# Kernel optimization log

Hardware: AMD Instinct MI355X
Metric: run time of the kernel (lower is better)

## Reference

```python
import jax, jax.numpy as jnp
import numpy as np
import math

D_MODEL = 512
D_STATE = 16
D_CONV = 4
EXPAND = 2
D_INNER = EXPAND * D_MODEL
DT_RANK = math.ceil(D_MODEL / 16)
B_SZ, L_SEQ = 4, 4096


def setup_inputs() -> dict:
    key = jax.random.key(0)
    ks = jax.random.split(key, 32)
    f32 = jnp.float32

    def nrm(k, shape, s=0.02):
        return (jax.random.normal(k, shape, dtype=f32) * s)

    # dt bias init (inverse softplus of dt in [dt_min, dt_max])
    def dt_bias(k):
        u = jax.random.uniform(k, (D_INNER,), dtype=f32)
        dt = jnp.exp(u * (math.log(0.1) - math.log(1e-3)) + math.log(1e-3))
        dt = jnp.clip(dt, 1e-4, None)
        return dt + jnp.log(-jnp.expm1(-dt))

    Alog = jnp.log(jnp.broadcast_to(jnp.arange(1, D_STATE + 1, dtype=f32), (D_INNER, D_STATE)))
    dt_std = DT_RANK ** (-0.5)

    inp = {
        'hidden_states': jax.random.normal(ks[0], (B_SZ, L_SEQ, D_MODEL), dtype=f32),
        'another_hidden_states': jax.random.normal(ks[1], (B_SZ, L_SEQ, D_MODEL), dtype=f32),
        'in_proj_w': nrm(ks[2], (2 * D_INNER, D_MODEL)),
        'in_proj_g_w': nrm(ks[3], (2 * D_INNER, D_MODEL)),
        'convw_f': nrm(ks[4], (D_INNER, D_CONV), 0.1),
        'convb_f': jnp.zeros((D_INNER,), f32),
        'convw_r': nrm(ks[5], (D_INNER, D_CONV), 0.1),
        'convb_r': jnp.zeros((D_INNER,), f32),
        'convw_g': nrm(ks[6], (D_INNER, D_CONV), 0.1),
        'convb_g': jnp.zeros((D_INNER,), f32),
        'xproj_f': nrm(ks[7], (DT_RANK + 2 * D_STATE, D_INNER)),
        'xproj_r': nrm(ks[8], (DT_RANK + 2 * D_STATE, D_INNER)),
        'xproj_g': nrm(ks[9], (DT_RANK + 2 * D_STATE, D_INNER)),
        'dtw_f': jax.random.uniform(ks[10], (D_INNER, DT_RANK), minval=-dt_std, maxval=dt_std, dtype=f32),
        'dtb_f': dt_bias(ks[11]),
        'dtw_r': jax.random.uniform(ks[12], (D_INNER, DT_RANK), minval=-dt_std, maxval=dt_std, dtype=f32),
        'dtb_r': dt_bias(ks[13]),
        'dtw_g': jax.random.uniform(ks[14], (D_INNER, DT_RANK), minval=-dt_std, maxval=dt_std, dtype=f32),
        'dtb_g': dt_bias(ks[15]),
        'Alog_f': Alog, 'Alog_r': Alog, 'Alog_g': Alog,
        'D_f': jnp.ones((D_INNER,), f32),
        'D_r': jnp.ones((D_INNER,), f32),
        'D_g': jnp.ones((D_INNER,), f32),
        'out_proj_w': nrm(ks[16], (D_MODEL, D_INNER)),
    }
    return inp


def _branch(xz, convw, convb, xproj, dtw, dtb, Alog, Dp):
    # xz: (B, L, 2*d_inner)
    b, l, _ = xz.shape
    d = xz.shape[-1] // 2
    x, z = xz[..., :d], xz[..., d:]
    # causal depthwise conv1d over L (pad left d_conv-1), then SiLU
    xc = jnp.transpose(x, (0, 2, 1))  # (B, d, L)
    xc = jax.lax.conv_general_dilated(
        xc, convw[:, None, :], (1,), [(convw.shape[-1] - 1, 0)],
        dimension_numbers=('NCH', 'OIH', 'NCH'), feature_group_count=d)
    xc = xc + convb[None, :, None]
    x = jax.nn.silu(jnp.transpose(xc, (0, 2, 1)))  # (B, L, d)
    # input-dependent dt, B, C
    dbl = x @ xproj.T  # (B, L, dt_rank + 2n)
    r = dtw.shape[1]
    n = Alog.shape[1]
    dt = jax.nn.softplus(dbl[..., :r] @ dtw.T + dtb)  # (B, L, d)
    Bs = dbl[..., r:r + n]   # (B, L, n)
    Cs = dbl[..., r + n:]    # (B, L, n)
    A = -jnp.exp(Alog)       # (d, n)

    def step(h, inp):
        dt_t, x_t, B_t, C_t = inp  # (B,d),(B,d),(B,n),(B,n)
        h = jnp.exp(dt_t[:, :, None] * A) * h + (dt_t * x_t)[:, :, None] * B_t[:, None, :]
        y = jnp.einsum('bdn,bn->bd', h, C_t)
        return h, y

    h0 = jnp.zeros((b, d, n), dtype=x.dtype)
    xs = (jnp.swapaxes(dt, 0, 1), jnp.swapaxes(x, 0, 1),
          jnp.swapaxes(Bs, 0, 1), jnp.swapaxes(Cs, 0, 1))
    _, ys = jax.lax.scan(step, h0, xs)
    y = jnp.swapaxes(ys, 0, 1) + Dp * x  # (B, L, d)
    return y * jax.nn.silu(z)


def reference(hidden_states, another_hidden_states, in_proj_w, in_proj_g_w,
              convw_f, convb_f, convw_r, convb_r, convw_g, convb_g,
              xproj_f, xproj_r, xproj_g,
              dtw_f, dtb_f, dtw_r, dtb_r, dtw_g, dtb_g,
              Alog_f, Alog_r, Alog_g, D_f, D_r, D_g, out_proj_w):
    xz = hidden_states @ in_proj_w.T           # (B, L, 2*d_inner)
    axz = another_hidden_states @ in_proj_g_w.T
    y_f = _branch(xz, convw_f, convb_f, xproj_f, dtw_f, dtb_f, Alog_f, D_f)
    y_r = jnp.flip(_branch(jnp.flip(xz, axis=1), convw_r, convb_r, xproj_r, dtw_r, dtb_r, Alog_r, D_r), axis=1)
    y_g = _branch(axz, convw_g, convb_g, xproj_g, dtw_g, dtb_g, Alog_g, D_g)
    out = ((y_f + y_r) * jax.nn.silu(y_g)) @ out_proj_w.T  # (B, L, d_model)
    return out
```

## Files before the change

kernel.cpp:

```cpp
#include <hip/hip_runtime.h>
#include <hip/hip_bf16.h>
#include <math.h>

#define L_SEQ 4096
#define B_SZ 4
#define D_MODEL 512
#define D_INNER 1024
#define DT_RANK 32
#define D_STATE 16
#define M_ROWS (B_SZ * L_SEQ)
#define NC 64
#define CHK (L_SEQ / NC)

typedef __hip_bfloat16 bf16;
typedef __bf16 bf16x8 __attribute__((ext_vector_type(8)));
typedef float f32x4 __attribute__((ext_vector_type(4)));
struct us8 { ushort4 a, b; };

__device__ __forceinline__ unsigned short f2us(float f) {
    union { bf16 h; unsigned short u; } t;
    t.h = __float2bfloat16(f);
    return t.u;
}
__device__ __forceinline__ float us2f(unsigned short u) {
    union { bf16 h; unsigned short u; } t;
    t.u = u;
    return __bfloat162float(t.h);
}

__device__ __forceinline__ float silu_f(float x) {
    const float xc = fminf(fmaxf(x, -60.0f), 60.0f);
    return x / (1.0f + __expf(-xc));
}
__device__ __forceinline__ float softplus_f(float x) {
    if (x > 20.0f) return x;
    if (x < -20.0f) return __expf(x);
    return log1pf(__expf(x));
}

struct CvtArgs {
    const float* src[9];
    unsigned short* dst[9];
    unsigned int vend[9];
    int nseg;
};
__global__ __launch_bounds__(256)
void cvt_multi(CvtArgs a)
{
    const unsigned int v = blockIdx.x * 256 + threadIdx.x;
    if (v >= a.vend[a.nseg - 1]) return;
    int s = 0;
    unsigned int vstart = 0;
    while (v >= a.vend[s]) { vstart = a.vend[s]; ++s; }
    const size_t lv = (size_t)(v - vstart) * 4;
    const float4 f = *(const float4*)(a.src[s] + lv);
    ushort4 o;
    o.x = f2us(f.x); o.y = f2us(f.y); o.z = f2us(f.z); o.w = f2us(f.w);
    *(ushort4*)(a.dst[s] + lv) = o;
}

template<int BM, int BN, int BK, int WY, int WX, int GATED, int EPI, int CT, int SWZ>
__global__ __launch_bounds__(256)
void gemm_mfma(const unsigned short* __restrict__ A,
               const unsigned short* __restrict__ A2,
               const unsigned short* __restrict__ W,
               const float* __restrict__ bias,
               void* __restrict__ Cp, unsigned short* __restrict__ C2p,
               int K, int lda, int ldb, int ldc)
{
    constexpr int CPR = BK / 8;
    constexpr int SWM = CPR - 1;
    constexpr int RPW = 64 / CPR;
    constexpr int NPA = BM / (4 * RPW);
    constexpr int NPB = BN / (4 * RPW);
    constexpr int WGX = BN / (WX * 16);
    static_assert(WGX * (BM / (WY * 16)) == 4, "4 waves");
    __shared__ unsigned short As[BM * BK];
    __shared__ unsigned short Bs[BN * BK];

    const int tid  = threadIdx.x;
    const int lane = tid & 63;
    const int wave = tid >> 6;
    const int wx = wave % WGX, wy = wave / WGX;
    const int l15 = lane & 15, quad = lane >> 4;

    int bid = blockIdx.y * gridDim.x + blockIdx.x;
    if (SWZ) {
        const int nwg = gridDim.x * gridDim.y;
        if ((nwg & 7) == 0) {
            const int cpx = nwg >> 3;
            bid = (bid & 7) * cpx + (bid >> 3);
        }
    }
    const int bxi = bid % gridDim.x;
    const int byi = bid / gridDim.x;
    const long row0 = (long)byi * BM;
    const long col0 = (long)bxi * BN;

    const int rin = lane / CPR;
    const int gc  = (lane % CPR) ^ (rin & SWM);

    f32x4 acc[WY][WX];
#pragma unroll
    for (int i = 0; i < WY; ++i)
#pragma unroll
        for (int j = 0; j < WX; ++j) acc[i][j] = (f32x4){0.f, 0.f, 0.f, 0.f};

    for (int k0 = 0; k0 < K; k0 += BK) {
        if (GATED == 0) {
#pragma unroll
            for (int p = 0; p < NPA; ++p) {
                const int rb = (p * 4 + wave) * RPW;
                const unsigned short* gp = A + (row0 + rb + rin) * (long)lda + k0 + gc * 8;
                const int lb = __builtin_amdgcn_readfirstlane(rb * BK);
                __builtin_amdgcn_global_load_lds(
                    (const __attribute__((address_space(1))) void*)gp,
                    (__attribute__((address_space(3))) void*)(As + lb), 16, 0, 0);
            }
        } else {
#pragma unroll
            for (int v = 0; v < BM * BK / 2048; ++v) {
                const int e = (v * 256 + tid) * 8;
                const int r = e / BK, c = (e % BK) / 8;
                const long off = (row0 + r) * (long)lda + k0 + c * 8;
                const us8 ta = *(const us8*)(A + off);
                const us8 tg = *(const us8*)(A2 + off);
                us8 t;
                t.a.x = f2us(us2f(ta.a.x) * silu_f(us2f(tg.a.x)));
                t.a.y = f2us(us2f(ta.a.y) * silu_f(us2f(tg.a.y)));
                t.a.z = f2us(us2f(ta.a.z) * silu_f(us2f(tg.a.z)));
                t.a.w = f2us(us2f(ta.a.w) * silu_f(us2f(tg.a.w)));
                t.b.x = f2us(us2f(ta.b.x) * silu_f(us2f(tg.b.x)));
                t.b.y = f2us(us2f(ta.b.y) * silu_f(us2f(tg.b.y)));
                t.b.z = f2us(us2f(ta.b.z) * silu_f(us2f(tg.b.z)));
                t.b.w = f2us(us2f(ta.b.w) * silu_f(us2f(tg.b.w)));
                *(us8*)&As[r * BK + ((c ^ (r & SWM)) * 8)] = t;
            }
        }
#pragma unroll
        for (int p = 0; p < NPB; ++p) {
            const int rb = (p * 4 + wave) * RPW;
            const unsigned short* gp = W + (col0 + rb + rin) * (long)ldb + k0 + gc * 8;
            const int lb = __builtin_amdgcn_readfirstlane(rb * BK);
            __builtin_amdgcn_global_load_lds(
                (const __attribute__((address_space(1))) void*)gp,
                (__attribute__((address_space(3))) void*)(Bs + lb), 16, 0, 0);
        }
        __syncthreads();

#pragma unroll
        for (int kk = 0; kk < BK / 32; ++kk) {
            bf16x8 aF[WY], bF[WX];
#pragma unroll
            for (int i = 0; i < WY; ++i) {
                const int r  = wy * WY * 16 + i * 16 + l15;
                const int kc = (kk * 4 + quad) ^ (r & SWM);
                aF[i] = *(const bf16x8*)&As[r * BK + kc * 8];
            }
#pragma unroll
            for (int j = 0; j < WX; ++j) {
                const int r  = wx * WX * 16 + j * 16 + l15;
                const int kc = (kk * 4 + quad) ^ (r & SWM);
                bF[j] = *(const bf16x8*)&Bs[r * BK + kc * 8];
            }
#pragma unroll
            for (int i = 0; i < WY; ++i)
#pragma unroll
                for (int j = 0; j < WX; ++j)
                    acc[i][j] = __builtin_amdgcn_mfma_f32_16x16x32_bf16(
                        aF[i], bF[j], acc[i][j], 0, 0, 0);
        }
        __syncthreads();
    }

#pragma unroll
    for (int i = 0; i < WY; ++i)
#pragma unroll
        for (int j = 0; j < WX; ++j) {
            const long mb = row0 + wy * WY * 16 + i * 16 + quad * 4;
            const long n  = col0 + wx * WX * 16 + j * 16 + l15;
            const float bv = (EPI == 1) ? bias[n] : 0.0f;
#pragma unroll
            for (int r = 0; r < 4; ++r) {
                float val = acc[i][j][r];
                if (EPI == 1) val = softplus_f(val + bv);
                const long off = (mb + r) * (long)ldc + n;
                if (CT == 0) ((unsigned short*)Cp)[off] = f2us(val);
                else         ((float*)Cp)[off] = val;
                if (EPI == 2 && n < DT_RANK) C2p[(mb + r) * DT_RANK + n] = f2us(val);
            }
        }
}

__global__ __launch_bounds__(256)
void conv_silu8(const unsigned short* __restrict__ xz, const float* __restrict__ w,
                const float* __restrict__ bias, unsigned short* __restrict__ xb, int rev)
{
    const int idx = blockIdx.x * 256 + threadIdx.x;
    const int g = idx & 127;
    const int m = idx >> 7;
    const int b = m >> 12;
    const int t = m & (L_SEQ - 1);
    const int d = g * 8;

    float s[8];
    {
        const float4 b0 = *(const float4*)(bias + d);
        const float4 b1 = *(const float4*)(bias + d + 4);
        s[0] = b0.x; s[1] = b0.y; s[2] = b0.z; s[3] = b0.w;
        s[4] = b1.x; s[5] = b1.y; s[6] = b1.z; s[7] = b1.w;
    }
    float4 wv[8];
#pragma unroll
    for (int j = 0; j < 8; ++j) wv[j] = *(const float4*)(w + (d + j) * 4);

    const unsigned short* xbase = xz + (size_t)b * L_SEQ * 2048 + d;
#pragma unroll
    for (int k = 0; k < 4; ++k) {
        const int src = t - 3 + k;
        if (src >= 0) {
            const int sm = rev ? (L_SEQ - 1 - src) : src;
            const us8 xv = *(const us8*)(xbase + (size_t)sm * 2048);
            const float tap[8] = {us2f(xv.a.x), us2f(xv.a.y), us2f(xv.a.z), us2f(xv.a.w),
                                  us2f(xv.b.x), us2f(xv.b.y), us2f(xv.b.z), us2f(xv.b.w)};
#pragma unroll
            for (int j = 0; j < 8; ++j) {
                const float wk = (k == 0) ? wv[j].x : (k == 1) ? wv[j].y
                               : (k == 2) ? wv[j].z : wv[j].w;
                s[j] = fmaf(wk, tap[j], s[j]);
            }
        }
    }
    us8 o;
    o.a.x = f2us(silu_f(s[0])); o.a.y = f2us(silu_f(s[1]));
    o.a.z = f2us(silu_f(s[2])); o.a.w = f2us(silu_f(s[3]));
    o.b.x = f2us(silu_f(s[4])); o.b.y = f2us(silu_f(s[5]));
    o.b.z = f2us(silu_f(s[6])); o.b.w = f2us(silu_f(s[7]));
    *(us8*)(xb + (size_t)m * 1024 + d) = o;
}

__device__ __forceinline__ bool a_struct_fast(const float* __restrict__ Alog,
                                              int d, float& A0)
{
    A0 = -__expf(Alog[d * 16]);
    bool fast = true;
#pragma unroll
    for (int n = 1; n < 16; ++n) {
        const float an = -__expf(Alog[d * 16 + n]);
        const float tg = (float)(n + 1) * A0;
        fast = fast && (fabsf(an - tg) <= 1e-5f * fabsf(tg));
    }
    return fast;
}
__device__ __forceinline__ void pow_tree16(float e1, float w[16])
{
    w[0] = e1;
    w[1] = w[0] * w[0];  w[2] = w[1] * w[0];  w[3] = w[1] * w[1];
    w[4] = w[3] * w[0];  w[5] = w[3] * w[1];  w[6] = w[3] * w[2];  w[7] = w[3] * w[3];
#pragma unroll
    for (int n = 8; n < 16; ++n) w[n] = w[7] * w[n - 8];
}

__global__ __launch_bounds__(512)
void scan_a(const unsigned short* __restrict__ dtq, const unsigned short* __restrict__ xq,
            const float* __restrict__ dbl, const float* __restrict__ Alog,
            float* __restrict__ hF, float* __restrict__ Ssum)
{
    const int tid = threadIdx.x;
    const int d = blockIdx.y * 512 + tid;
    const int c = blockIdx.x;
    const int b = blockIdx.z;

    __shared__ float Bsh[CHK][16];
    for (int e = tid; e < CHK * 16; e += 512)
        Bsh[e >> 4][e & 15] = dbl[((size_t)b * L_SEQ + c * CHK + (e >> 4)) * 64 + DT_RANK + (e & 15)];
    __syncthreads();

    float A0;
    const bool fast = a_struct_fast(Alog, d, A0);

    float h[16];
#pragma unroll
    for (int n = 0; n < 16; ++n) h[n] = 0.0f;
    float S = 0.0f;

    const size_t base = ((size_t)b * L_SEQ + c * CHK) * 1024 + d;
    const unsigned short* dtp = dtq + base;
    const unsigned short* xp  = xq + base;

    if (fast) {
        unsigned short bd[4], bx[4];
#pragma unroll
        for (int i = 0; i < 4; ++i) {
            bd[i] = dtp[(size_t)i * 1024];
            bx[i] = xp[(size_t)i * 1024];
        }
        for (int t0 = 0; t0 < CHK; t0 += 4) {
            unsigned short nd[4], nx[4];
            const bool pf = (t0 + 4 < CHK);
            if (pf) {
#pragma unroll
                for (int i = 0; i < 4; ++i) {
                    nd[i] = dtp[(size_t)(t0 + 4 + i) * 1024];
                    nx[i] = xp[(size_t)(t0 + 4 + i) * 1024];
                }
            }
#pragma unroll
            for (int i = 0; i < 4; ++i) {
                const float dt = us2f(bd[i]);
                const float xv = us2f(bx[i]);
                S += dt;
                const float dtx = dt * xv;
                float w[16];
                pow_tree16(__expf(dt * A0), w);
#pragma unroll
                for (int n = 0; n < 16; ++n)
                    h[n] = fmaf(w[n], h[n], dtx * Bsh[t0 + i][n]);
            }
            if (pf) {
#pragma unroll
                for (int i = 0; i < 4; ++i) { bd[i] = nd[i]; bx[i] = nx[i]; }
            }
        }
    } else {
        float Acoef[16];
#pragma unroll
        for (int n = 0; n < 16; ++n) Acoef[n] = -__expf(Alog[d * 16 + n]);
        unsigned short vd = dtp[0], vx = xp[0];
        for (int t = 0; t < CHK; ++t) {
            unsigned short vd2 = 0, vx2 = 0;
            if (t + 1 < CHK) {
                vd2 = dtp[(size_t)(t + 1) * 1024];
                vx2 = xp[(size_t)(t + 1) * 1024];
            }
            const float dt = us2f(vd);
            const float xv = us2f(vx);
            S += dt;
            const float dtx = dt * xv;
#pragma unroll
            for (int n = 0; n < 16; ++n)
                h[n] = fmaf(__expf(dt * Acoef[n]), h[n], dtx * Bsh[t][n]);
            vd = vd2; vx = vx2;
        }
    }

    float* hp = hF + (((size_t)(b * NC + c) * 1024 + d) << 4);
#pragma unroll
    for (int n = 0; n < 16; ++n) hp[n] = h[n];
    Ssum[(size_t)(b * NC + c) * 1024 + d] = S;
}

__global__ __launch_bounds__(256)
void scan_b(float* __restrict__ hF, const float* __restrict__ Ssum,
            const float* __restrict__ Alog)
{
    const int idx = blockIdx.x * 256 + threadIdx.x;
    const int n  = idx & 15;
    const int dn = idx >> 4;
    const int d  = dn & (D_INNER - 1);
    const int b  = dn >> 10;

    const float Acoef = -__expf(Alog[d * 16 + n]);
    float H = 0.0f;
    for (int c = 0; c < NC; ++c) {
        const size_t base = (size_t)(b * NC + c) * 1024 + d;
        const float S = Ssum[base];
        float* hp = hF + (base << 4) + n;
        const float hOld = *hp;
        *hp = H;
        H = fmaf(__expf(Acoef * S), H, hOld);
    }
}

__global__ __launch_bounds__(512)
void scan_c(const unsigned short* __restrict__ dtq, const unsigned short* __restrict__ xq,
            const float* __restrict__ dbl, const float* __restrict__ hF,
            const float* __restrict__ Alog, const float* __restrict__ Dp,
            const unsigned short* __restrict__ xz, unsigned short* __restrict__ yout,
            const unsigned short* __restrict__ gate, int rev, int acc)
{
    const int tid = threadIdx.x;
    const int d = blockIdx.y * 512 + tid;
    const int c = blockIdx.x;
    const int b = blockIdx.z;

    __shared__ float Bsh[CHK][16];
    __shared__ float Csh[CHK][16];
    for (int e = tid; e < CHK * 16; e += 512) {
        const size_t rb = ((size_t)b * L_SEQ + c * CHK + (e >> 4)) * 64;
        Bsh[e >> 4][e & 15] = dbl[rb + DT_RANK + (e & 15)];
        Csh[e >> 4][e & 15] = dbl[rb + DT_RANK + D_STATE + (e & 15)];
    }
    __syncthreads();

    float A0;
    const bool fast = a_struct_fast(Alog, d, A0);
    const float Dd = Dp[d];

    float h[16];
    {
        const float* hp = hF + (((size_t)(b * NC + c) * 1024 + d) << 4);
#pragma unroll
        for (int n = 0; n < 16; ++n) h[n] = hp[n];
    }

    const size_t base = ((size_t)b * L_SEQ + c * CHK) * 1024 + d;
    const unsigned short* dtp = dtq + base;
    const unsigned short* xp  = xq + base;
    const unsigned short* z_base = xz + (size_t)b * L_SEQ * 2048 + D_INNER + d;
    const unsigned short* g_base = gate ? gate + (size_t)b * L_SEQ * D_INNER + d : nullptr;
    unsigned short* y_base = yout + (size_t)b * L_SEQ * D_INNER + d;

    if (fast) {
        unsigned short bd[4], bx[4], bz[4], bg[4];
#pragma unroll
        for (int i = 0; i < 4; ++i) {
            bd[i] = dtp[(size_t)i * 1024];
            bx[i] = xp[(size_t)i * 1024];
            const int tg = c * CHK + i;
            const int tm = rev ? (L_SEQ - 1 - tg) : tg;
            bz[i] = z_base[(size_t)tm * 2048];
            bg[i] = g_base ? g_base[(size_t)tm * D_INNER] : (unsigned short)0;
        }
        for (int t0 = 0; t0 < CHK; t0 += 4) {
            unsigned short nd[4], nx[4], nz[4], ng[4];
            const bool pf = (t0 + 4 < CHK);
            if (pf) {
#pragma unroll
                for (int i = 0; i < 4; ++i) {
                    nd[i] = dtp[(size_t)(t0 + 4 + i) * 1024];
                    nx[i] = xp[(size_t)(t0 + 4 + i) * 1024];
                    const int tg = c * CHK + t0 + 4 + i;
                    const int tm = rev ? (L_SEQ - 1 - tg) : tg;
                    nz[i] = z_base[(size_t)tm * 2048];
                    ng[i] = g_base ? g_base[(size_t)tm * D_INNER] : (unsigned short)0;
                }
            }
#pragma unroll
            for (int i = 0; i < 4; ++i) {
                const float dt = us2f(bd[i]);
                const float xv = us2f(bx[i]);
                const float dtx = dt * xv;
                float w[16];
                pow_tree16(__expf(dt * A0), w);
                float y = 0.0f;
#pragma unroll
                for (int n = 0; n < 16; ++n) {
                    h[n] = fmaf(w[n], h[n], dtx * Bsh[t0 + i][n]);
                    y = fmaf(h[n], Csh[t0 + i][n], y);
                }
                const int tg = c * CHK + t0 + i;
                const int tm = rev ? (L_SEQ - 1 - tg) : tg;
                const float z = us2f(bz[i]);
                float yo = (y + Dd * xv) * silu_f(z);
                const size_t oi = (size_t)tm * D_INNER;
                if (acc) yo += us2f(y_base[oi]);
                if (g_base) yo *= silu_f(us2f(bg[i]));
                y_base[oi] = f2us(yo);
            }
            if (pf) {
#pragma unroll
                for (int i = 0; i < 4; ++i) { bd[i] = nd[i]; bx[i] = nx[i]; bz[i] = nz[i]; bg[i] = ng[i]; }
            }
        }
    } else {
        float Acoef[16];
#pragma unroll
        for (int n = 0; n < 16; ++n) Acoef[n] = -__expf(Alog[d * 16 + n]);
        unsigned short vd = dtp[0], vx = xp[0];
        for (int t = 0; t < CHK; ++t) {
            unsigned short vd2 = 0, vx2 = 0;
            if (t + 1 < CHK) {
                vd2 = dtp[(size_t)(t + 1) * 1024];
                vx2 = xp[(size_t)(t + 1) * 1024];
            }
            const float dt = us2f(vd);
            const float xv = us2f(vx);
            const float dtx = dt * xv;
            float y = 0.0f;
#pragma unroll
            for (int n = 0; n < 16; ++n) {
                h[n] = fmaf(__expf(dt * Acoef[n]), h[n], dtx * Bsh[t][n]);
                y = fmaf(h[n], Csh[t][n], y);
            }
            const int tg = c * CHK + t;
            const int tm = rev ? (L_SEQ - 1 - tg) : tg;
            const float z = us2f(z_base[(size_t)tm * 2048]);
            float yo = (y + Dd * xv) * silu_f(z);
            const size_t oi = (size_t)tm * D_INNER;
            if (acc) yo += us2f(y_base[oi]);
            if (g_base) yo *= silu_f(us2f(g_base[oi]));
            y_base[oi] = f2us(yo);
            vd = vd2; vx = vx2;
        }
    }
}

extern "C" void kernel_launch(void* const* d_in, const int* in_sizes, int n_in,
                              void* d_out, int out_size, void* d_ws, size_t ws_size,
                              hipStream_t stream)
{
    const float* hs    = (const float*)d_in[0];
    const float* ahs   = (const float*)d_in[1];
    const float* in_w  = (const float*)d_in[2];
    const float* in_gw = (const float*)d_in[3];
    const float* convw[3] = {(const float*)d_in[4], (const float*)d_in[6], (const float*)d_in[8]};
    const float* convb[3] = {(const float*)d_in[5], (const float*)d_in[7], (const float*)d_in[9]};
    const float* xproj[3] = {(const float*)d_in[10], (const float*)d_in[11], (const float*)d_in[12]};
    const float* dtw[3]   = {(const float*)d_in[13], (const float*)d_in[15], (const float*)d_in[17]};
    const float* dtbias[3]= {(const float*)d_in[14], (const float*)d_in[16], (const float*)d_in[18]};
    const float* Alog[3]  = {(const float*)d_in[19], (const float*)d_in[20], (const float*)d_in[21]};
    const float* Dp[3]    = {(const float*)d_in[22], (const float*)d_in[23], (const float*)d_in[24]};
    const float* out_w = (const float*)d_in[25];

    unsigned short* regA = (unsigned short*)d_ws;
    float* dbl  = (float*)(regA + (size_t)M_ROWS * 2048);
    unsigned short* xb  = (unsigned short*)(dbl + (size_t)M_ROWS * 64);
    unsigned short* dtv = xb  + (size_t)M_ROWS * 1024;
    unsigned short* yfr = dtv + (size_t)M_ROWS * 1024;
    unsigned short* yg  = yfr + (size_t)M_ROWS * 1024;
    float* hF   = (float*)(yg + (size_t)M_ROWS * 1024);
    float* Ssum = hF + (size_t)B_SZ * NC * 1024 * 16;
    unsigned short* dtin = (unsigned short*)(Ssum + (size_t)B_SZ * NC * 1024);
    unsigned short* wbig = dtin + (size_t)M_ROWS * 32;
    unsigned short* wout = wbig + (size_t)2048 * 512;
    unsigned short* wxpb = wout + (size_t)512 * 1024;
    unsigned short* wdtb = wxpb + (size_t)3 * 64 * 1024;
    unsigned short* inb  = yfr;

    const dim3 blk(256);

    {
        CvtArgs a;
        unsigned int acc = 0;
        const float* srcs[9] = {ahs, in_gw, out_w, xproj[0], xproj[1], xproj[2],
                                dtw[0], dtw[1], dtw[2]};
        unsigned short* dsts[9] = {inb, wbig, wout,
                                   wxpb, wxpb + 64 * 1024, wxpb + 2 * 64 * 1024,
                                   wdtb, wdtb + 1024 * 32, wdtb + 2 * 1024 * 32};
        const unsigned int sz[9] = {M_ROWS * 512u, 2048u * 512u, 512u * 1024u,
                                    64u * 1024u, 64u * 1024u, 64u * 1024u,
                                    1024u * 32u, 1024u * 32u, 1024u * 32u};
        for (int i = 0; i < 9; ++i) {
            a.src[i] = srcs[i]; a.dst[i] = dsts[i];
            acc += sz[i] / 4; a.vend[i] = acc;
        }
        a.nseg = 9;
        cvt_multi<<<dim3((acc + 255) / 256), blk, 0, stream>>>(a);
    }

    const int order[3] = {2, 0, 1};

    gemm_mfma<128,128,64,4,4,0,0,0,1><<<dim3(16, 128), blk, 0, stream>>>(
        inb, nullptr, wbig, nullptr, regA, nullptr, D_MODEL, D_MODEL, D_MODEL, 2048);

    for (int oi = 0; oi < 3; ++oi) {
        const int br = order[oi];
        const int rev  = (br == 1) ? 1 : 0;
        const int accf = (br == 1) ? 1 : 0;
        unsigned short* ybuf = (br == 2) ? yg : yfr;
        const unsigned short* gatep = (br == 1) ? yg : nullptr;

        if (br == 0) {
            CvtArgs a;
            a.src[0] = hs;   a.dst[0] = inb;  a.vend[0] = M_ROWS * 512u / 4;
            a.src[1] = in_w; a.dst[1] = wbig; a.vend[1] = a.vend[0] + 2048u * 512u / 4;
            a.nseg = 2;
            cvt_multi<<<dim3((a.vend[1] + 255) / 256), blk, 0, stream>>>(a);
            gemm_mfma<128,128,64,4,4,0,0,0,1><<<dim3(16, 128), blk, 0, stream>>>(
                inb, nullptr, wbig, nullptr, regA, nullptr, D_MODEL, D_MODEL, D_MODEL, 2048);
        }

        conv_silu8<<<dim3(M_ROWS * 128 / 256), blk, 0, stream>>>(
            regA, convw[br], convb[br], xb, rev);

        gemm_mfma<64,64,64,2,2,0,2,1,0><<<dim3(1, 256), blk, 0, stream>>>(
            xb, nullptr, wxpb + br * 64 * 1024, nullptr, dbl, dtin,
            D_INNER, D_INNER, D_INNER, 64);

        gemm_mfma<128,128,32,4,4,0,1,0,0><<<dim3(8, 128), blk, 0, stream>>>(
            dtin, nullptr, wdtb + br * 1024 * 32, dtbias[br], dtv, nullptr,
            DT_RANK, DT_RANK, DT_RANK, D_INNER);

        scan_a<<<dim3(NC, 2, B_SZ), dim3(512), 0, stream>>>(dtv, xb, dbl, Alog[br], hF, Ssum);
        scan_b<<<dim3((B_SZ * D_INNER * 16) / 256), blk, 0, stream>>>(hF, Ssum, Alog[br]);
        scan_c<<<dim3(NC, 2, B_SZ), dim3(512), 0, stream>>>(
            dtv, xb, dbl, hF, Alog[br], Dp[br], regA, ybuf, gatep, rev, accf);
    }

    gemm_mfma<128,128,64,4,4,0,0,1,0><<<dim3(4, 128), blk, 0, stream>>>(
        yfr, nullptr, wout, nullptr, d_out, nullptr, D_INNER, D_INNER, D_INNER, D_MODEL);
}
```

Measured before the change: 980.4 us.

## Split SSM scan state across thread pairs to double parallelism

The scan_a and scan_c kernels now assign each channel to two threads, each owning eight of the sixteen state entries, with blocks raised to 1024 threads. Power weights for the upper half are built by multiplying by e^8, and the output dot product is combined with a lane shuffle before one lane writes. This is meant to cut per-thread register pressure and serial work, and to raise occupancy and latency hiding for the memory-bound scan. In exchange, dt, x, z and gate loads are duplicated across paired lanes and a shuffle is added at every timestep.

```diff
diff --git a/kernel.cpp b/kernel.cpp
--- a/kernel.cpp
+++ b/kernel.cpp
@@ -252,36 +252,39 @@
     }
     return fast;
 }
-__device__ __forceinline__ void pow_tree16(float e1, float w[16])
-{
-    w[0] = e1;
-    w[1] = w[0] * w[0];  w[2] = w[1] * w[0];  w[3] = w[1] * w[1];
-    w[4] = w[3] * w[0];  w[5] = w[3] * w[1];  w[6] = w[3] * w[2];  w[7] = w[3] * w[3];
-#pragma unroll
-    for (int n = 8; n < 16; ++n) w[n] = w[7] * w[n - 8];
-}
-
-__global__ __launch_bounds__(512)
+__device__ __forceinline__ void pow_half8(float e1, float wb_sel, float w[8])
+{
+    const float p1 = e1;
+    const float p2 = p1 * p1, p3 = p2 * p1, p4 = p2 * p2;
+    const float p5 = p4 * p1, p6 = p4 * p2, p7 = p4 * p3, p8 = p4 * p4;
+    const float wb = wb_sel ? p8 : 1.0f;
+    w[0] = wb * p1; w[1] = wb * p2; w[2] = wb * p3; w[3] = wb * p4;
+    w[4] = wb * p5; w[5] = wb * p6; w[6] = wb * p7; w[7] = wb * p8;
+}
+
+__global__ __launch_bounds__(1024, 8)
 void scan_a(const unsigned short* __restrict__ dtq, const unsigned short* __restrict__ xq,
             const float* __restrict__ dbl, const float* __restrict__ Alog,
             float* __restrict__ hF, float* __restrict__ Ssum)
 {
     const int tid = threadIdx.x;
-    const int d = blockIdx.y * 512 + tid;
+    const int nh  = tid & 1;
+    const int d   = blockIdx.y * 512 + (tid >> 1);
+    const int nb  = nh * 8;
     const int c = blockIdx.x;
     const int b = blockIdx.z;
 
     __shared__ float Bsh[CHK][16];
-    for (int e = tid; e < CHK * 16; e += 512)
-        Bsh[e >> 4][e & 15] = dbl[((size_t)b * L_SEQ + c * CHK + (e >> 4)) * 64 + DT_RANK + (e & 15)];
+    Bsh[tid >> 4][tid & 15] =
+        dbl[((size_t)b * L_SEQ + c * CHK + (tid >> 4)) * 64 + DT_RANK + (tid & 15)];
     __syncthreads();
 
     float A0;
     const bool fast = a_struct_fast(Alog, d, A0);
 
-    float h[16];
-#pragma unroll
-    for (int n = 0; n < 16; ++n) h[n] = 0.0f;
+    float h[8];
+#pragma unroll
+    for (int k = 0; k < 8; ++k) h[k] = 0.0f;
     float S = 0.0f;
 
     const size_t base = ((size_t)b * L_SEQ + c * CHK) * 1024 + d;
@@ -311,11 +314,11 @@
                 const float xv = us2f(bx[i]);
                 S += dt;
                 const float dtx = dt * xv;
-                float w[16];
-                pow_tree16(__expf(dt * A0), w);
-#pragma unroll
-                for (int n = 0; n < 16; ++n)
-                    h[n] = fmaf(w[n], h[n], dtx * Bsh[t0 + i][n]);
+                float w[8];
+                pow_half8(__expf(dt * A0), (float)nh, w);
+#pragma unroll
+                for (int k = 0; k < 8; ++k)
+                    h[k] = fmaf(w[k], h[k], dtx * Bsh[t0 + i][nb + k]);
             }
             if (pf) {
 #pragma unroll
@@ -323,9 +326,9 @@
             }
         }
     } else {
-        float Acoef[16];
-#pragma unroll
-        for (int n = 0; n < 16; ++n) Acoef[n] = -__expf(Alog[d * 16 + n]);
+        float Acoef[8];
+#pragma unroll
+        for (int k = 0; k < 8; ++k) Acoef[k] = -__expf(Alog[d * 16 + nb + k]);
         unsigned short vd = dtp[0], vx = xp[0];
         for (int t = 0; t < CHK; ++t) {
             unsigned short vd2 = 0, vx2 = 0;
@@ -338,16 +341,16 @@
             S += dt;
             const float dtx = dt * xv;
 #pragma unroll
-            for (int n = 0; n < 16; ++n)
-                h[n] = fmaf(__expf(dt * Acoef[n]), h[n], dtx * Bsh[t][n]);
+            for (int k = 0; k < 8; ++k)
+                h[k] = fmaf(__expf(dt * Acoef[k]), h[k], dtx * Bsh[t][nb + k]);
             vd = vd2; vx = vx2;
         }
     }
 
-    float* hp = hF + (((size_t)(b * NC + c) * 1024 + d) << 4);
-#pragma unroll
-    for (int n = 0; n < 16; ++n) hp[n] = h[n];
-    Ssum[(size_t)(b * NC + c) * 1024 + d] = S;
+    float* hp = hF + ((((size_t)(b * NC + c) * 1024 + d) << 4) + nb);
+#pragma unroll
+    for (int k = 0; k < 8; ++k) hp[k] = h[k];
+    if (nh == 0) Ssum[(size_t)(b * NC + c) * 1024 + d] = S;
 }
 
 __global__ __launch_bounds__(256)
@@ -372,7 +375,7 @@
     }
 }
 
-__global__ __launch_bounds__(512)
+__global__ __launch_bounds__(1024, 8)
 void scan_c(const unsigned short* __restrict__ dtq, const unsigned short* __restrict__ xq,
             const float* __restrict__ dbl, const float* __restrict__ hF,
             const float* __restrict__ Alog, const float* __restrict__ Dp,
@@ -380,16 +383,18 @@
             const unsigned short* __restrict__ gate, int rev, int acc)
 {
     const int tid = threadIdx.x;
-    const int d = blockIdx.y * 512 + tid;
+    const int nh  = tid & 1;
+    const int d   = blockIdx.y * 512 + (tid >> 1);
+    const int nb  = nh * 8;
     const int c = blockIdx.x;
     const int b = blockIdx.z;
 
     __shared__ float Bsh[CHK][16];
     __shared__ float Csh[CHK][16];
-    for (int e = tid; e < CHK * 16; e += 512) {
-        const size_t rb = ((size_t)b * L_SEQ + c * CHK + (e >> 4)) * 64;
-        Bsh[e >> 4][e & 15] = dbl[rb + DT_RANK + (e & 15)];
-        Csh[e >> 4][e & 15] = dbl[rb + DT_RANK + D_STATE + (e & 15)];
+    {
+        const size_t rb = ((size_t)b * L_SEQ + c * CHK + (tid >> 4)) * 64;
+        Bsh[tid >> 4][tid & 15] = dbl[rb + DT_RANK + (tid & 15)];
+        Csh[tid >> 4][tid & 15] = dbl[rb + DT_RANK + D_STATE + (tid & 15)];
     }
     __syncthreads();
 
@@ -397,11 +402,11 @@
     const bool fast = a_struct_fast(Alog, d, A0);
     const float Dd = Dp[d];
 
-    float h[16];
+    float h[8];
     {
-        const float* hp = hF + (((size_t)(b * NC + c) * 1024 + d) << 4);
-#pragma unroll
-        for (int n = 0; n < 16; ++n) h[n] = hp[n];
+        const float* hp = hF + ((((size_t)(b * NC + c) * 1024 + d) << 4) + nb);
+#pragma unroll
+        for (int k = 0; k < 8; ++k) h[k] = hp[k];
     }
 
     const size_t base = ((size_t)b * L_SEQ + c * CHK) * 1024 + d;
@@ -441,14 +446,15 @@
                 const float dt = us2f(bd[i]);
                 const float xv = us2f(bx[i]);
                 const float dtx = dt * xv;
-                float w[16];
-                pow_tree16(__expf(dt * A0), w);
+                float w[8];
+                pow_half8(__expf(dt * A0), (float)nh, w);
                 float y = 0.0f;
 #pragma unroll
-                for (int n = 0; n < 16; ++n) {
-                    h[n] = fmaf(w[n], h[n], dtx * Bsh[t0 + i][n]);
-                    y = fmaf(h[n], Csh[t0 + i][n], y);
+                for (int k = 0; k < 8; ++k) {
+                    h[k] = fmaf(w[k], h[k], dtx * Bsh[t0 + i][nb + k]);
+                    y = fmaf(h[k], Csh[t0 + i][nb + k], y);
                 }
+                y += __shfl_xor(y, 1);
                 const int tg = c * CHK + t0 + i;
                 const int tm = rev ? (L_SEQ - 1 - tg) : tg;
                 const float z = us2f(bz[i]);
@@ -456,7 +462,7 @@
                 const size_t oi = (size_t)tm * D_INNER;
                 if (acc) yo += us2f(y_base[oi]);
                 if (g_base) yo *= silu_f(us2f(bg[i]));
-                y_base[oi] = f2us(yo);
+                if (nh == 0) y_base[oi] = f2us(yo);
             }
             if (pf) {
 #pragma unroll
@@ -464,9 +470,9 @@
             }
         }
     } else {
-        float Acoef[16];
-#pragma unroll
-        for (int n = 0; n < 16; ++n) Acoef[n] = -__expf(Alog[d * 16 + n]);
+        float Acoef[8];
+#pragma unroll
+        for (int k = 0; k < 8; ++k) Acoef[k] = -__expf(Alog[d * 16 + nb + k]);
         unsigned short vd = dtp[0], vx = xp[0];
         for (int t = 0; t < CHK; ++t) {
             unsigned short vd2 = 0, vx2 = 0;
@@ -479,10 +485,11 @@
             const float dtx = dt * xv;
             float y = 0.0f;
 #pragma unroll
-            for (int n = 0; n < 16; ++n) {
-                h[n] = fmaf(__expf(dt * Acoef[n]), h[n], dtx * Bsh[t][n]);
-                y = fmaf(h[n], Csh[t][n], y);
-            }
+            for (int k = 0; k < 8; ++k) {
+                h[k] = fmaf(__expf(dt * Acoef[k]), h[k], dtx * Bsh[t][nb + k]);
+                y = fmaf(h[k], Csh[t][nb + k], y);
+            }
+            y += __shfl_xor(y, 1);
             const int tg = c * CHK + t;
             const int tm = rev ? (L_SEQ - 1 - tg) : tg;
             const float z = us2f(z_base[(size_t)tm * 2048]);
@@ -490,7 +497,7 @@
             const size_t oi = (size_t)tm * D_INNER;
             if (acc) yo += us2f(y_base[oi]);
             if (g_base) yo *= silu_f(us2f(g_base[oi]));
-            y_base[oi] = f2us(yo);
+            if (nh == 0) y_base[oi] = f2us(yo);
             vd = vd2; vx = vx2;
         }
     }
@@ -582,9 +589,9 @@
             dtin, nullptr, wdtb + br * 1024 * 32, dtbias[br], dtv, nullptr,
             DT_RANK, DT_RANK, DT_RANK, D_INNER);
 
-        scan_a<<<dim3(NC, 2, B_SZ), dim3(512), 0, stream>>>(dtv, xb, dbl, Alog[br], hF, Ssum);
+        scan_a<<<dim3(NC, 2, B_SZ), dim3(1024), 0, stream>>>(dtv, xb, dbl, Alog[br], hF, Ssum);
         scan_b<<<dim3((B_SZ * D_INNER * 16) / 256), blk, 0, stream>>>(hF, Ssum, Alog[br]);
-        scan_c<<<dim3(NC, 2, B_SZ), dim3(512), 0, stream>>>(
+        scan_c<<<dim3(NC, 2, B_SZ), dim3(1024), 0, stream>>>(
             dtv, xb, dbl, hF, Alog[br], Dp[br], regA, ybuf, gatep, rev, accf);
     }
 
```

Result: slower. 1.226 ms (+25.0%).
